# Kernel optimization log

Measured on AMD Instinct MI355X. Metric: run time of the kernel, lower is better.

## Reference

```python
import jax, jax.numpy as jnp
import numpy as np
from jax import lax

EPS = 1e-5


def setup_inputs() -> dict:
    key = jax.random.key(0)
    ks = jax.random.split(key, 6)
    n, c, t, v, K = 64, 256, 64, 25, 3
    c4 = c // 4
    x = jax.random.normal(ks[0], (n, c, t, v), dtype=jnp.float32)
    # G branch: Linear(t -> 2t, no bias), BN1d(2t), Linear(2t -> K, no bias)
    Wg1 = jax.random.normal(ks[1], (2 * t, t), dtype=jnp.float32) * 0.1
    gamma1 = jnp.ones((2 * t,), jnp.float32)
    beta1 = jnp.zeros((2 * t,), jnp.float32)
    mean1 = jnp.zeros((2 * t,), jnp.float32)
    var1 = jnp.ones((2 * t,), jnp.float32)
    Wg2 = jax.random.normal(ks[2], (K, 2 * t), dtype=jnp.float32) * 0.1
    # L branch: Conv1d(c -> c/4, k=3, pad=1, no bias), BN1d(c/4), Conv1d(c/4 -> c, k=1, no bias)
    WL1 = jax.random.normal(ks[3], (c4, c, K), dtype=jnp.float32) * 0.05
    gamma2 = jnp.ones((c4,), jnp.float32)
    beta2 = jnp.zeros((c4,), jnp.float32)
    mean2 = jnp.zeros((c4,), jnp.float32)
    var2 = jnp.ones((c4,), jnp.float32)
    WL2 = jax.random.normal(ks[4], (c, c4, 1), dtype=jnp.float32) * 0.05
    return {"x": x, "Wg1": Wg1, "gamma1": gamma1, "beta1": beta1, "mean1": mean1,
            "var1": var1, "Wg2": Wg2, "WL1": WL1, "gamma2": gamma2, "beta2": beta2,
            "mean2": mean2, "var2": var2, "WL2": WL2}


def _bn(h, gamma, beta, mean, var):
    return (h - mean) * gamma * lax.rsqrt(var + EPS) + beta


def reference(x, Wg1, gamma1, beta1, mean1, var1, Wg2, WL1, gamma2, beta2, mean2, var2, WL2):
    n, c, t, v = x.shape
    K = Wg2.shape[0]
    pad = 1  # module default padding (temporal)
    # adaptive_avg_pool2d(x, (t, 1)) == mean over joints v -> (n, c, t)
    pooled = x.mean(axis=-1)
    # --- G: per-(n,c) temporal kernel via MLP + softmax ---
    h = pooled.reshape(n * c, t) @ Wg1.T                  # (n*c, 2t)
    h = jax.nn.relu(_bn(h, gamma1, beta1, mean1, var1))
    kern = jax.nn.softmax(h @ Wg2.T, axis=-1)             # (n*c, K)
    kern = kern.reshape(n, c, K)
    # --- L: channel-wise local activation (conv1d over t) ---
    dn = ('NCH', 'OIH', 'NCH')
    a = lax.conv_general_dilated(pooled, WL1, (1,), [(K // 2, K // 2)], dimension_numbers=dn)
    a = jax.nn.relu(_bn(a, gamma2[None, :, None], beta2[None, :, None],
                        mean2[None, :, None], var2[None, :, None]))
    a = lax.conv_general_dilated(a, WL2, (1,), [(0, 0)], dimension_numbers=dn)
    act = jax.nn.sigmoid(a)                               # (n, c, t)
    new_x = x * act[..., None]                            # (n, c, t, v)
    # --- dynamic depthwise temporal conv (groups = n*c) ---
    xp = jnp.pad(new_x, ((0, 0), (0, 0), (pad, pad), (0, 0)))
    out = jnp.zeros_like(x)
    for k in range(K):  # K is tiny (3)
        out = out + kern[:, :, k, None, None] * xp[:, :, k:k + t, :]
    return out + x
```

## Files before the change

### kernel.cpp

```cpp
#include <hip/hip_runtime.h>
#include <math.h>

#define EPSB 1e-5f

constexpr int N_ = 64, C_ = 256, T_ = 64, V_ = 25, C4_ = 64;
constexpr int NC = N_ * C_;
constexpr int TV = T_ * V_;

__global__ __launch_bounds__(256) void k_pool(const float* __restrict__ x,
                                              float* __restrict__ pooled) {
    __shared__ float xs[4 * TV];
    const int b = blockIdx.x;
    const float4* xp4 = (const float4*)(x + (size_t)b * (4 * TV));
    float4* xs4 = (float4*)xs;
    for (int f = threadIdx.x; f < TV; f += 256) xs4[f] = xp4[f];
    __syncthreads();
    float s = 0.f;
    const int base = threadIdx.x * V_;
#pragma unroll
    for (int v = 0; v < V_; ++v) s += xs[base + v];
    pooled[(size_t)b * 256 + threadIdx.x] = s * (1.0f / 25.0f);
}

__global__ __launch_bounds__(256) void k_gbranch(
    const float* __restrict__ pooled, const float* __restrict__ Wg1,
    const float* __restrict__ g1, const float* __restrict__ b1,
    const float* __restrict__ m1, const float* __restrict__ v1,
    const float* __restrict__ Wg2, float* __restrict__ kern) {
    __shared__ float Wt[T_ * 130];
    for (int e = threadIdx.x; e < 128 * T_; e += 256) {
        const int j = e >> 6, t = e & 63;
        Wt[t * 130 + j] = Wg1[e];
    }
    __syncthreads();

    const int lane = threadIdx.x & 63;
    const int gw = blockIdx.x * 4 + (threadIdx.x >> 6);
    const int j0 = lane, j1 = lane + 64;

    float w0[T_], w1[T_];
#pragma unroll
    for (int t = 0; t < T_; ++t) {
        w0[t] = Wt[t * 130 + j0];
        w1[t] = Wt[t * 130 + j1];
    }
    const float s0 = g1[j0] * rsqrtf(v1[j0] + EPSB);
    const float s1 = g1[j1] * rsqrtf(v1[j1] + EPSB);
    const float c0 = b1[j0] - m1[j0] * s0;
    const float c1 = b1[j1] - m1[j1] * s1;
    const float wa0 = Wg2[0 * 128 + j0], wa1 = Wg2[0 * 128 + j1];
    const float wb0 = Wg2[1 * 128 + j0], wb1 = Wg2[1 * 128 + j1];
    const float wc0 = Wg2[2 * 128 + j0], wc1 = Wg2[2 * 128 + j1];

    for (int rr = 0; rr < 8; ++rr) {
        const int row = __builtin_amdgcn_readfirstlane(gw * 8 + rr);
        const float* __restrict__ prow = pooled + (size_t)row * T_;
        float h0 = 0.f, h1 = 0.f;
#pragma unroll
        for (int t = 0; t < T_; ++t) {
            const float pt = prow[t];
            h0 = fmaf(w0[t], pt, h0);
            h1 = fmaf(w1[t], pt, h1);
        }
        h0 = fmaxf(fmaf(h0, s0, c0), 0.f);
        h1 = fmaxf(fmaf(h1, s1, c1), 0.f);
        float p0 = wa0 * h0 + wa1 * h1;
        float p1 = wb0 * h0 + wb1 * h1;
        float p2 = wc0 * h0 + wc1 * h1;
#pragma unroll
        for (int off = 32; off > 0; off >>= 1) {
            p0 += __shfl_xor(p0, off);
            p1 += __shfl_xor(p1, off);
            p2 += __shfl_xor(p2, off);
        }
        const float mx = fmaxf(p0, fmaxf(p1, p2));
        const float e0 = expf(p0 - mx), e1 = expf(p1 - mx), e2 = expf(p2 - mx);
        const float inv = 1.0f / (e0 + e1 + e2);
        if (lane < 3) {
            const float val = (lane == 0) ? e0 : (lane == 1) ? e1 : e2;
            kern[(size_t)row * 3 + lane] = val * inv;
        }
    }
}

__global__ __launch_bounds__(256) void kL1(
    const float* __restrict__ pooled, const float* __restrict__ WL1,
    const float* __restrict__ g2, const float* __restrict__ b2,
    const float* __restrict__ m2, const float* __restrict__ v2,
    float* __restrict__ a1) {
    __shared__ float ps[C_ * 66];
    const int n = blockIdx.x >> 2;
    const int bq = blockIdx.x & 3;
    const int w = threadIdx.x >> 6;
    const int t = threadIdx.x & 63;
    const float* pn = pooled + (size_t)n * (C_ * T_);

    for (int e = threadIdx.x; e < C_ * T_; e += 256) {
        const int i = e >> 6, tt = e & 63;
        ps[i * 66 + 1 + tt] = pn[e];
    }
    {
        const int i = threadIdx.x;
        ps[i * 66] = 0.f;
        ps[i * 66 + 65] = 0.f;
    }
    __syncthreads();

    const int ccb = __builtin_amdgcn_readfirstlane(bq * 16 + w * 4);
    const float* __restrict__ wb = WL1 + (size_t)ccb * (C_ * 3);
    float a0 = 0.f, a1v = 0.f, a2 = 0.f, a3 = 0.f;
#pragma unroll 4
    for (int i = 0; i < C_; ++i) {
        const float pm = ps[i * 66 + t];
        const float pc = ps[i * 66 + 1 + t];
        const float pp = ps[i * 66 + 2 + t];
        a0 = fmaf(wb[0 * 768 + i * 3 + 0], pm, fmaf(wb[0 * 768 + i * 3 + 1], pc, fmaf(wb[0 * 768 + i * 3 + 2], pp, a0)));
        a1v = fmaf(wb[1 * 768 + i * 3 + 0], pm, fmaf(wb[1 * 768 + i * 3 + 1], pc, fmaf(wb[1 * 768 + i * 3 + 2], pp, a1v)));
        a2 = fmaf(wb[2 * 768 + i * 3 + 0], pm, fmaf(wb[2 * 768 + i * 3 + 1], pc, fmaf(wb[2 * 768 + i * 3 + 2], pp, a2)));
        a3 = fmaf(wb[3 * 768 + i * 3 + 0], pm, fmaf(wb[3 * 768 + i * 3 + 1], pc, fmaf(wb[3 * 768 + i * 3 + 2], pp, a3)));
    }
    float* ab = a1 + ((size_t)n * C4_ + ccb) * T_ + t;
    const float acc[4] = {a0, a1v, a2, a3};
#pragma unroll
    for (int j = 0; j < 4; ++j) {
        const int cc = ccb + j;
        const float sc = g2[cc] * rsqrtf(v2[cc] + EPSB);
        const float sh = b2[cc] - m2[cc] * sc;
        ab[j * T_] = fmaxf(fmaf(acc[j], sc, sh), 0.f);
    }
}

__global__ __launch_bounds__(256) void kL2(
    const float* __restrict__ a1, const float* __restrict__ WL2,
    float* __restrict__ act) {
    const int n = blockIdx.x >> 4;
    const int bq = blockIdx.x & 15;
    const int w = threadIdx.x >> 6;
    const int t = threadIdx.x & 63;
    const int cb = __builtin_amdgcn_readfirstlane(bq * 16 + w * 4);
    const float* __restrict__ an = a1 + (size_t)n * (C4_ * T_);
    const float* __restrict__ w2 = WL2 + (size_t)cb * C4_;
    float o0 = 0.f, o1 = 0.f, o2 = 0.f, o3 = 0.f;
#pragma unroll 4
    for (int i = 0; i < C4_; ++i) {
        const float av = an[i * T_ + t];
        o0 = fmaf(w2[0 * C4_ + i], av, o0);
        o1 = fmaf(w2[1 * C4_ + i], av, o1);
        o2 = fmaf(w2[2 * C4_ + i], av, o2);
        o3 = fmaf(w2[3 * C4_ + i], av, o3);
    }
    float* ar = act + ((size_t)n * C_ + cb) * T_ + t;
    ar[0 * T_] = 1.0f / (1.0f + expf(-o0));
    ar[1 * T_] = 1.0f / (1.0f + expf(-o1));
    ar[2 * T_] = 1.0f / (1.0f + expf(-o2));
    ar[3 * T_] = 1.0f / (1.0f + expf(-o3));
}

__global__ __launch_bounds__(256) void k_final(const float* __restrict__ x,
                                               const float* __restrict__ act,
                                               const float* __restrict__ kern,
                                               float* __restrict__ out) {
    __shared__ float xs[TV];
    __shared__ float as[T_ + 2];
    const int row = blockIdx.x;
    const float4* xr4 = (const float4*)(x + (size_t)row * TV);
    float4* outr4 = (float4*)(out + (size_t)row * TV);
    float4* xs4 = (float4*)xs;
    for (int f = threadIdx.x; f < TV / 4; f += 256) xs4[f] = xr4[f];
    if (threadIdx.x < T_ + 2) {
        const int t = (int)threadIdx.x - 1;
        as[threadIdx.x] = (t >= 0 && t < T_) ? act[(size_t)row * T_ + t] : 0.f;
    }
    const float k0 = kern[(size_t)row * 3 + 0];
    const float k1 = kern[(size_t)row * 3 + 1];
    const float k2 = kern[(size_t)row * 3 + 2];
    __syncthreads();
    for (int f = threadIdx.x; f < TV / 4; f += 256) {
        float r[4];
#pragma unroll
        for (int q = 0; q < 4; ++q) {
            const int e = f * 4 + q;
            const int t = e / 25;
            const float xc = xs[e];
            const float xm = (t > 0)  ? xs[e - 25] : 0.f;
            const float xq = (t < 63) ? xs[e + 25] : 0.f;
            r[q] = xc + k0 * xm * as[t] + k1 * xc * as[t + 1] + k2 * xq * as[t + 2];
        }
        outr4[f] = make_float4(r[0], r[1], r[2], r[3]);
    }
}

extern "C" void kernel_launch(void* const* d_in, const int* in_sizes, int n_in,
                              void* d_out, int out_size, void* d_ws, size_t ws_size,
                              hipStream_t stream) {
    const float* x   = (const float*)d_in[0];
    const float* Wg1 = (const float*)d_in[1];
    const float* g1  = (const float*)d_in[2];
    const float* b1  = (const float*)d_in[3];
    const float* m1  = (const float*)d_in[4];
    const float* v1  = (const float*)d_in[5];
    const float* Wg2 = (const float*)d_in[6];
    const float* WL1 = (const float*)d_in[7];
    const float* g2  = (const float*)d_in[8];
    const float* b2  = (const float*)d_in[9];
    const float* m2  = (const float*)d_in[10];
    const float* v2  = (const float*)d_in[11];
    const float* WL2 = (const float*)d_in[12];
    float* out = (float*)d_out;

    float* ws = (float*)d_ws;
    float* pooled = ws;
    float* act    = ws + (size_t)NC * T_;
    float* kern   = ws + (size_t)2 * NC * T_;
    float* a1buf  = ws + (size_t)2 * NC * T_ + (size_t)NC * 4;

    k_pool   <<<NC / 4, 256, 0, stream>>>(x, pooled);
    k_gbranch<<<512,    256, 0, stream>>>(pooled, Wg1, g1, b1, m1, v1, Wg2, kern);
    kL1      <<<N_ * 4, 256, 0, stream>>>(pooled, WL1, g2, b2, m2, v2, a1buf);
    kL2      <<<N_ * 16,256, 0, stream>>>(a1buf, WL2, act);
    k_final  <<<NC,     256, 0, stream>>>(x, act, kern, out);
}
```

Before: 279.3 us.

## Fuse all stages into one cooperative persistent kernel with grid syncs

Replaces five separate kernel launches with a single cooperative persistent kernel that runs pooling, then the G-branch MLP and L-branch convolutions concurrently on different block roles, then the final depthwise conv, separated by grid.sync(). The G-branch now batches 8 rows per wave using readlane broadcasts, and the L-branch fuses both 1D convs through shared memory, so the intermediate a1 buffer disappears. This removes launch gaps and the a1 round trip to global memory. In exchange it adds grid-wide barrier cost and uneven load between roles. The final stage now reads x directly from global memory without staging it in shared memory, and uses scalar stores instead of float4.

```diff
diff --git a/kernel.cpp b/kernel.cpp
--- a/kernel.cpp
+++ b/kernel.cpp
@@ -1,11 +1,191 @@
 #include <hip/hip_runtime.h>
+#include <hip/hip_cooperative_groups.h>
 #include <math.h>
+
+namespace cg = cooperative_groups;
 
 #define EPSB 1e-5f
 
 constexpr int N_ = 64, C_ = 256, T_ = 64, V_ = 25, C4_ = 64;
 constexpr int NC = N_ * C_;
 constexpr int TV = T_ * V_;
+
+union SMemU {
+    float pool[4 * TV];
+    float Wt[64 * 130];
+    struct { float ps[C_ * 18]; float a1s[C4_ * 17]; } L;
+};
+
+__global__ __launch_bounds__(256, 4) void kfused(
+    const float* __restrict__ x, const float* __restrict__ Wg1,
+    const float* __restrict__ g1, const float* __restrict__ b1,
+    const float* __restrict__ m1, const float* __restrict__ v1,
+    const float* __restrict__ Wg2, const float* __restrict__ WL1,
+    const float* __restrict__ g2, const float* __restrict__ b2,
+    const float* __restrict__ m2, const float* __restrict__ v2,
+    const float* __restrict__ WL2, float* __restrict__ out,
+    float* __restrict__ pooled, float* __restrict__ act,
+    float* __restrict__ kern) {
+    __shared__ SMemU sm;
+    const int tid = threadIdx.x;
+    const int bid = blockIdx.x;
+    const int nB = gridDim.x;
+    cg::grid_group grid = cg::this_grid();
+
+    for (int g = bid; g < NC / 4; g += nB) {
+        const float4* xp4 = (const float4*)(x + (size_t)g * (4 * TV));
+        float4* s4 = (float4*)sm.pool;
+        for (int f = tid; f < TV; f += 256) s4[f] = xp4[f];
+        __syncthreads();
+        float s = 0.f;
+        const int base = tid * 25;
+#pragma unroll
+        for (int v = 0; v < 25; ++v) s += sm.pool[base + v];
+        pooled[(size_t)g * 256 + tid] = s * (1.0f / 25.0f);
+        __syncthreads();
+    }
+    grid.sync();
+
+    const int role = bid & 3;
+    const int lane = tid & 63;
+    const int wv = tid >> 6;
+    if (role < 3) {
+        for (int e = tid; e < 128 * 64; e += 256) {
+            const int j = e >> 6, t = e & 63;
+            sm.Wt[t * 130 + j] = Wg1[e];
+        }
+        __syncthreads();
+        const int j0 = lane, j1 = lane + 64;
+        const float s0 = g1[j0] * rsqrtf(v1[j0] + EPSB);
+        const float s1 = g1[j1] * rsqrtf(v1[j1] + EPSB);
+        const float c0 = b1[j0] - m1[j0] * s0;
+        const float c1 = b1[j1] - m1[j1] * s1;
+        const float wa0 = Wg2[j0], wa1 = Wg2[j1];
+        const float wb0 = Wg2[128 + j0], wb1 = Wg2[128 + j1];
+        const float wc0 = Wg2[256 + j0], wc1 = Wg2[256 + j1];
+        const int Gbid = (bid >> 2) * 3 + role;
+        const int gwid = Gbid * 4 + wv;
+        const int nGw = (nB >> 2) * 12;
+        for (int ch = gwid; ch < NC / 8; ch += nGw) {
+            const int r0 = ch * 8;
+            float pv[8], h0[8], h1[8];
+#pragma unroll
+            for (int r = 0; r < 8; ++r) {
+                pv[r] = pooled[(size_t)(r0 + r) * 64 + lane];
+                h0[r] = 0.f; h1[r] = 0.f;
+            }
+#pragma unroll
+            for (int tb = 0; tb < 4; ++tb) {
+                float w0[16], w1[16];
+#pragma unroll
+                for (int tt = 0; tt < 16; ++tt) {
+                    w0[tt] = sm.Wt[(tb * 16 + tt) * 130 + j0];
+                    w1[tt] = sm.Wt[(tb * 16 + tt) * 130 + j1];
+                }
+#pragma unroll
+                for (int tt = 0; tt < 16; ++tt) {
+#pragma unroll
+                    for (int r = 0; r < 8; ++r) {
+                        const float pt = __uint_as_float(
+                            __builtin_amdgcn_readlane(__float_as_uint(pv[r]), tb * 16 + tt));
+                        h0[r] = fmaf(w0[tt], pt, h0[r]);
+                        h1[r] = fmaf(w1[tt], pt, h1[r]);
+                    }
+                }
+            }
+#pragma unroll
+            for (int r = 0; r < 8; ++r) {
+                const float a0 = fmaxf(fmaf(h0[r], s0, c0), 0.f);
+                const float a1v = fmaxf(fmaf(h1[r], s1, c1), 0.f);
+                float p0 = wa0 * a0 + wa1 * a1v;
+                float p1 = wb0 * a0 + wb1 * a1v;
+                float p2 = wc0 * a0 + wc1 * a1v;
+#pragma unroll
+                for (int off = 32; off > 0; off >>= 1) {
+                    p0 += __shfl_xor(p0, off);
+                    p1 += __shfl_xor(p1, off);
+                    p2 += __shfl_xor(p2, off);
+                }
+                const float mx = fmaxf(p0, fmaxf(p1, p2));
+                const float e0 = expf(p0 - mx), e1 = expf(p1 - mx), e2 = expf(p2 - mx);
+                const float inv = 1.0f / (e0 + e1 + e2);
+                if (lane < 3) {
+                    const float val = (lane == 0) ? e0 : (lane == 1) ? e1 : e2;
+                    kern[(size_t)(r0 + r) * 3 + lane] = val * inv;
+                }
+            }
+        }
+    } else {
+        const int Lbid = bid >> 2;
+        for (int tile = Lbid; tile < 256; tile += (nB >> 2)) {
+            const int n = tile >> 2;
+            const int t0 = (tile & 3) * 16;
+            for (int e = tid; e < C_ * 18; e += 256) {
+                const int i = e / 18, tt = e - i * 18;
+                const int gt = t0 - 1 + tt;
+                sm.L.ps[e] = (gt >= 0 && gt < 64)
+                                 ? pooled[(size_t)n * 16384 + i * 64 + gt] : 0.f;
+            }
+            __syncthreads();
+            const int tg = lane >> 4;
+            const int t = lane & 15;
+            const int ccb = wv * 16;
+            float acc[4] = {0.f, 0.f, 0.f, 0.f};
+            for (int i = 0; i < C_; ++i) {
+                const float pm = sm.L.ps[i * 18 + t];
+                const float pc = sm.L.ps[i * 18 + t + 1];
+                const float pp = sm.L.ps[i * 18 + t + 2];
+#pragma unroll
+                for (int q = 0; q < 4; ++q) {
+                    const float* wr = WL1 + (size_t)(ccb + q * 4 + tg) * 768 + i * 3;
+                    acc[q] = fmaf(wr[0], pm, fmaf(wr[1], pc, fmaf(wr[2], pp, acc[q])));
+                }
+            }
+#pragma unroll
+            for (int q = 0; q < 4; ++q) {
+                const int cc = ccb + q * 4 + tg;
+                const float sc = g2[cc] * rsqrtf(v2[cc] + EPSB);
+                const float sh = b2[cc] - m2[cc] * sc;
+                sm.L.a1s[cc * 17 + t] = fmaxf(fmaf(acc[q], sc, sh), 0.f);
+            }
+            __syncthreads();
+            const int c = tid;
+            float o[16];
+#pragma unroll
+            for (int q = 0; q < 16; ++q) o[q] = 0.f;
+            const float* w2 = WL2 + (size_t)c * 64;
+            for (int i = 0; i < 64; ++i) {
+                const float w = w2[i];
+#pragma unroll
+                for (int q = 0; q < 16; ++q) o[q] = fmaf(w, sm.L.a1s[i * 17 + q], o[q]);
+            }
+            float* ar = act + ((size_t)n * 256 + c) * 64 + t0;
+#pragma unroll
+            for (int q = 0; q < 16; ++q) ar[q] = 1.0f / (1.0f + expf(-o[q]));
+            __syncthreads();
+        }
+    }
+    grid.sync();
+
+    for (int row = bid; row < NC; row += nB) {
+        const float* xr = x + (size_t)row * TV;
+        const float* acr = act + (size_t)row * 64;
+        float* outr = out + (size_t)row * TV;
+        const float k0 = kern[(size_t)row * 3 + 0];
+        const float k1 = kern[(size_t)row * 3 + 1];
+        const float k2 = kern[(size_t)row * 3 + 2];
+        for (int e = tid; e < TV; e += 256) {
+            const int t = e / 25;
+            const float xc = xr[e];
+            const float xm = (t > 0) ? xr[e - 25] : 0.f;
+            const float xq = (t < 63) ? xr[e + 25] : 0.f;
+            const float am = (t > 0) ? acr[t - 1] : 0.f;
+            const float ac = acr[t];
+            const float ap = (t < 63) ? acr[t + 1] : 0.f;
+            outr[e] = fmaf(k0, xm * am, fmaf(k1, xc * ac, fmaf(k2, xq * ap, xc)));
+        }
+    }
+}
 
 __global__ __launch_bounds__(256) void k_pool(const float* __restrict__ x,
                                               float* __restrict__ pooled) {
@@ -33,11 +213,9 @@
         Wt[t * 130 + j] = Wg1[e];
     }
     __syncthreads();
-
     const int lane = threadIdx.x & 63;
     const int gw = blockIdx.x * 4 + (threadIdx.x >> 6);
     const int j0 = lane, j1 = lane + 64;
-
     float w0[T_], w1[T_];
 #pragma unroll
     for (int t = 0; t < T_; ++t) {
@@ -48,10 +226,9 @@
     const float s1 = g1[j1] * rsqrtf(v1[j1] + EPSB);
     const float c0 = b1[j0] - m1[j0] * s0;
     const float c1 = b1[j1] - m1[j1] * s1;
-    const float wa0 = Wg2[0 * 128 + j0], wa1 = Wg2[0 * 128 + j1];
-    const float wb0 = Wg2[1 * 128 + j0], wb1 = Wg2[1 * 128 + j1];
-    const float wc0 = Wg2[2 * 128 + j0], wc1 = Wg2[2 * 128 + j1];
-
+    const float wa0 = Wg2[j0], wa1 = Wg2[j1];
+    const float wb0 = Wg2[128 + j0], wb1 = Wg2[128 + j1];
+    const float wc0 = Wg2[256 + j0], wc1 = Wg2[256 + j1];
     for (int rr = 0; rr < 8; ++rr) {
         const int row = __builtin_amdgcn_readfirstlane(gw * 8 + rr);
         const float* __restrict__ prow = pooled + (size_t)row * T_;
@@ -94,7 +271,6 @@
     const int w = threadIdx.x >> 6;
     const int t = threadIdx.x & 63;
     const float* pn = pooled + (size_t)n * (C_ * T_);
-
     for (int e = threadIdx.x; e < C_ * T_; e += 256) {
         const int i = e >> 6, tt = e & 63;
         ps[i * 66 + 1 + tt] = pn[e];
@@ -105,7 +281,6 @@
         ps[i * 66 + 65] = 0.f;
     }
     __syncthreads();
-
     const int ccb = __builtin_amdgcn_readfirstlane(bq * 16 + w * 4);
     const float* __restrict__ wb = WL1 + (size_t)ccb * (C_ * 3);
     float a0 = 0.f, a1v = 0.f, a2 = 0.f, a3 = 0.f;
@@ -120,13 +295,13 @@
         a3 = fmaf(wb[3 * 768 + i * 3 + 0], pm, fmaf(wb[3 * 768 + i * 3 + 1], pc, fmaf(wb[3 * 768 + i * 3 + 2], pp, a3)));
     }
     float* ab = a1 + ((size_t)n * C4_ + ccb) * T_ + t;
-    const float acc[4] = {a0, a1v, a2, a3};
+    const float accv[4] = {a0, a1v, a2, a3};
 #pragma unroll
     for (int j = 0; j < 4; ++j) {
         const int cc = ccb + j;
         const float sc = g2[cc] * rsqrtf(v2[cc] + EPSB);
         const float sh = b2[cc] - m2[cc] * sc;
-        ab[j * T_] = fmaxf(fmaf(acc[j], sc, sh), 0.f);
+        ab[j * T_] = fmaxf(fmaf(accv[j], sc, sh), 0.f);
     }
 }
 
@@ -182,7 +357,7 @@
             const int e = f * 4 + q;
             const int t = e / 25;
             const float xc = xs[e];
-            const float xm = (t > 0)  ? xs[e - 25] : 0.f;
+            const float xm = (t > 0) ? xs[e - 25] : 0.f;
             const float xq = (t < 63) ? xs[e + 25] : 0.f;
             r[q] = xc + k0 * xm * as[t] + k1 * xc * as[t + 1] + k2 * xq * as[t + 2];
         }
@@ -214,9 +389,25 @@
     float* kern   = ws + (size_t)2 * NC * T_;
     float* a1buf  = ws + (size_t)2 * NC * T_ + (size_t)NC * 4;
 
-    k_pool   <<<NC / 4, 256, 0, stream>>>(x, pooled);
-    k_gbranch<<<512,    256, 0, stream>>>(pooled, Wg1, g1, b1, m1, v1, Wg2, kern);
-    kL1      <<<N_ * 4, 256, 0, stream>>>(pooled, WL1, g2, b2, m2, v2, a1buf);
-    kL2      <<<N_ * 16,256, 0, stream>>>(a1buf, WL2, act);
-    k_final  <<<NC,     256, 0, stream>>>(x, act, kern, out);
-}
+    int nb = 0;
+    hipError_t oe = hipOccupancyMaxActiveBlocksPerMultiprocessor(&nb, kfused, 256, 0);
+    int grid = (oe == hipSuccess && nb >= 1) ? nb * 256 : 768;
+    if (grid > 1024) grid = 1024;
+    grid &= ~3;
+    if (grid < 4) grid = 4;
+
+    void* args[] = {(void*)&x,  (void*)&Wg1, (void*)&g1, (void*)&b1,
+                    (void*)&m1, (void*)&v1,  (void*)&Wg2, (void*)&WL1,
+                    (void*)&g2, (void*)&b2,  (void*)&m2, (void*)&v2,
+                    (void*)&WL2, (void*)&out, (void*)&pooled, (void*)&act,
+                    (void*)&kern};
+    hipError_t le = hipLaunchCooperativeKernel((void*)kfused, dim3(grid), dim3(256),
+                                               args, 0, stream);
+    if (le != hipSuccess) {
+        k_pool   <<<NC / 4, 256, 0, stream>>>(x, pooled);
+        k_gbranch<<<512,    256, 0, stream>>>(pooled, Wg1, g1, b1, m1, v1, Wg2, kern);
+        kL1      <<<N_ * 4, 256, 0, stream>>>(pooled, WL1, g2, b2, m2, v2, a1buf);
+        kL2      <<<N_ * 16, 256, 0, stream>>>(a1buf, WL2, act);
+        k_final  <<<NC,     256, 0, stream>>>(x, act, kern, out);
+    }
+}
```

New measurement: 546.7 us. 95.7% more time.
